# Performance work log

Hardware: AMD Instinct MI355X
Metric: run time of the kernel (lower is better)

Reference implementation:

```python
import jax, jax.numpy as jnp
import numpy as np

S, B, D, H, K, M, MEM = 1024, 2, 1024, 16, 64, 4096, 1
T = (MEM + 1) * S  # key length = (mem_len+1)*seq_len


def setup_inputs() -> dict:
    key = jax.random.key(0)
    ks = jax.random.split(key, 16)

    def w(k, shape):  # N(0, 0.02) init as in the torch module
        return jax.random.normal(k, shape, dtype=jnp.float32) * 0.02

    x = jax.random.normal(ks[0], (S, B, D), dtype=jnp.float32)
    p = jax.random.normal(ks[1], (T, B, D), dtype=jnp.float32)
    memory = jax.random.normal(ks[2], (MEM * S, B, D), dtype=jnp.float32)
    u_bias = w(ks[3], (H, K))
    v_bias = w(ks[4], (H, K))
    # Transformer-XL causal mask: query s may attend to keys t <= mem_len*S + s
    t_idx = jnp.arange(T)[None, :]
    s_idx = jnp.arange(S)[:, None]
    mask = jnp.where(t_idx <= MEM * S + s_idx, 0.0, -1e9).astype(jnp.float32)[None]  # [1,S,T]
    return {
        "x": x, "p": p, "mask": mask, "memory": memory,
        "u_bias": u_bias, "v_bias": v_bias,
        "wq_w": w(ks[5], (H * K, D)), "wke_w": w(ks[6], (H * K, D)),
        "wkr_w": w(ks[7], (H * K, D)), "wv_w": w(ks[8], (H * K, D)),
        "wc_w": w(ks[9], (D, H * K)),
        "w1_w": w(ks[10], (M, D)), "w1_b": jnp.zeros((M,), jnp.float32),
        "w2_w": w(ks[11], (D, M)), "w2_b": jnp.zeros((D,), jnp.float32),
        "ln1_g": jnp.ones((D,), jnp.float32), "ln1_b": jnp.zeros((D,), jnp.float32),
        "ln2_g": jnp.ones((D,), jnp.float32), "ln2_b": jnp.zeros((D,), jnp.float32),
    }


def _layernorm(x, g, b, eps=1e-5):
    mu = jnp.mean(x, axis=-1, keepdims=True)
    var = jnp.mean(jnp.square(x - mu), axis=-1, keepdims=True)
    return (x - mu) / jnp.sqrt(var + eps) * g + b


def reference(x, p, mask, memory, u_bias, v_bias,
              wq_w, wke_w, wkr_w, wv_w, wc_w,
              w1_w, w1_b, w2_w, w2_b, ln1_g, ln1_b, ln2_g, ln2_b):
    s_len, b_sz, d = x.shape
    q = (x @ wq_w.T).reshape(s_len, b_sz, H, K)            # [S,B,H,K]
    x_mem = jnp.concatenate([memory, x], axis=0)           # [T,B,D]
    k_e = (x_mem @ wke_w.T).reshape(T, b_sz, H, K)         # content keys
    k_r = (p @ wkr_w.T).reshape(T, b_sz, H, K)             # relative-position keys
    v = (x_mem @ wv_w.T).reshape(T, b_sz, H, K)
    # AC: content score, BD: relative-position score (Transformer-XL)
    ac = jnp.einsum("sbhk,tbhk->bhst", q + u_bias, k_e)
    bd = jnp.einsum("sbhk,tbhk->bhst", q + v_bias, k_r)
    alpha = (ac + bd) / np.sqrt(K).astype(np.float32) + mask[:, None]  # [B,H,S,T]
    alpha = jax.nn.softmax(alpha, axis=-1)
    av = jnp.einsum("bhst,tbhk->sbhk", alpha, v).reshape(s_len, b_sz, H * K)
    u = av @ wc_w.T
    u = _layernorm(u + x, ln1_g, ln1_b)
    z = jax.nn.relu(u @ w1_w.T + w1_b) @ w2_w.T + w2_b
    z = _layernorm(z + u, ln2_g, ln2_b)
    return z
```

## Files before the change

kernel.cpp:

```cpp
#include <hip/hip_runtime.h>
#include <math.h>

#define S_LEN 1024
#define BATCH 2
#define DM 1024
#define NH 16
#define HD 64
#define FFN_DIM 4096
#define T_LEN 2048
#define RQ 2048
#define RT 4096
#define KROW 72

typedef __attribute__((ext_vector_type(8))) short short8;
typedef __attribute__((ext_vector_type(4))) float f32x4;

__device__ __forceinline__ unsigned short f2bf(float f) {
    unsigned u = __builtin_bit_cast(unsigned, f);
    u += 0x7fffu + ((u >> 16) & 1u);
    return (unsigned short)(u >> 16);
}
__device__ __forceinline__ float bf2f(unsigned short s) { return __builtin_bit_cast(float, ((unsigned)s) << 16); }

#define GLD_LDS16(gptr, lptr)                                                                  \
    __builtin_amdgcn_global_load_lds((const __attribute__((address_space(1))) unsigned int*)(gptr), \
                                     (__attribute__((address_space(3))) unsigned int*)(lptr), 16, 0, 0)

__device__ __forceinline__ ushort4 cvt4(float4 v) {
    ushort4 o;
    o.x = f2bf(v.x); o.y = f2bf(v.y); o.z = f2bf(v.z); o.w = f2bf(v.w);
    return o;
}

__global__ void cast_all_kernel(const float* __restrict__ wq, const float* __restrict__ wke,
                                const float* __restrict__ wv, const float* __restrict__ wkr,
                                const float* __restrict__ wc, const float* __restrict__ w1,
                                const float* __restrict__ w2, const float* __restrict__ x,
                                const float* __restrict__ p, const float* __restrict__ mem,
                                unsigned short* __restrict__ wdst, unsigned short* __restrict__ xbf,
                                unsigned short* __restrict__ pbf, unsigned short* __restrict__ xm) {
    const long Q = 256 * 1024;
    const long W = 13 * Q;
    long i = (long)blockIdx.x * blockDim.x + threadIdx.x;
    if (i < W) {
        const float* src; long off;
        if      (i < 1 * Q) { src = wq;  off = 0; }
        else if (i < 2 * Q) { src = wke; off = 1 * Q; }
        else if (i < 3 * Q) { src = wv;  off = 2 * Q; }
        else if (i < 4 * Q) { src = wkr; off = 3 * Q; }
        else if (i < 5 * Q) { src = wc;  off = 4 * Q; }
        else if (i < 9 * Q) { src = w1;  off = 5 * Q; }
        else                { src = w2;  off = 9 * Q; }
        ((ushort4*)wdst)[i] = cvt4(((const float4*)src)[i - off]);
    } else if (i < W + 2 * Q) {
        long j = i - W;
        ((ushort4*)xbf)[j] = cvt4(((const float4*)x)[j]);
    } else if (i < W + 6 * Q) {
        long j = i - W - 2 * Q;
        ((ushort4*)pbf)[j] = cvt4(((const float4*)p)[j]);
    } else {
        long j = i - W - 6 * Q;
        float4 v = (j < 2 * Q) ? ((const float4*)mem)[j] : ((const float4*)x)[j - 2 * Q];
        ((ushort4*)xm)[j] = cvt4(v);
    }
}

#define BM 128
#define BN 64
#define BK 32

__launch_bounds__(256)
__global__ void proj_fused(const unsigned short* __restrict__ xbf, const unsigned short* __restrict__ xmbf,
                           const unsigned short* __restrict__ pbf, const unsigned short* __restrict__ wqb,
                           const unsigned short* __restrict__ wkevb, const unsigned short* __restrict__ wkrb,
                           unsigned short* __restrict__ qo, unsigned short* __restrict__ keo,
                           unsigned short* __restrict__ vTo, unsigned short* __restrict__ kro) {
    __shared__ __align__(16) short As[BM * BK];
    __shared__ __align__(16) short Bs[BN * BK];
    const int id = blockIdx.x;
    const unsigned short *A, *B;
    unsigned short *Yb, *Yv = nullptr;
    int bx, by;
    if (id < 256)       { A = xbf;  B = wqb;   Yb = qo;  bx = id & 15;  by = id >> 4; }
    else if (id < 1280) { int t = id - 256;  A = xmbf; B = wkevb; Yb = keo; Yv = vTo;
                          bx = t & 31; by = t >> 5; }
    else                { int t = id - 1280; A = pbf;  B = wkrb;  Yb = kro;
                          bx = t & 15; by = t >> 4; }
    const int tid = threadIdx.x;
    const int w = tid >> 6, lane = tid & 63;
    const int row0 = by * BM, col0 = bx * BN;
    const int wr = (w >> 1) * 64, wcn = (w & 1) * 32;
    f32x4 acc[4][2] = {};
    const int lrow = lane & 15, quad = lane >> 4;
    for (int k0 = 0; k0 < DM; k0 += BK) {
        __syncthreads();
#pragma unroll
        for (int i = 0; i < 2; ++i) {
            int c = w * 128 + i * 64 + lane;
            int row = c >> 2, kg = c & 3;
            int kl = (kg - (row >> 1)) & 3;
            GLD_LDS16(A + (long)(row0 + row) * DM + k0 + kl * 8, As + (w * 128 + i * 64) * 8);
        }
        {
            int row = tid >> 2, kg = tid & 3;
            int kl = (kg - (row >> 1)) & 3;
            GLD_LDS16(B + (long)(col0 + row) * DM + k0 + kl * 8, Bs + (w * 64) * 8);
        }
        __syncthreads();
        short8 a[4], b[2];
#pragma unroll
        for (int mi = 0; mi < 4; ++mi) {
            int r = wr + mi * 16 + lrow;
            int ph = (quad + (r >> 1)) & 3;
            a[mi] = *(const short8*)&As[r * BK + ph * 8];
        }
#pragma unroll
        for (int ni = 0; ni < 2; ++ni) {
            int r = wcn + ni * 16 + lrow;
            int ph = (quad + (r >> 1)) & 3;
            b[ni] = *(const short8*)&Bs[r * BK + ph * 8];
        }
#pragma unroll
        for (int mi = 0; mi < 4; ++mi)
#pragma unroll
            for (int ni = 0; ni < 2; ++ni)
                acc[mi][ni] = __builtin_amdgcn_mfma_f32_16x16x32_bf16(a[mi], b[ni], acc[mi][ni], 0, 0, 0);
    }
    const int mb = row0 + wr + quad * 4;
    const int nb = col0 + wcn + lrow;
    const bool iske = (col0 < 1024);
#pragma unroll
    for (int mi = 0; mi < 4; ++mi)
#pragma unroll
        for (int ni = 0; ni < 2; ++ni) {
            const int r = mb + mi * 16, cc = nb + ni * 16;
#pragma unroll
            for (int reg = 0; reg < 4; ++reg) {
                float val = acc[mi][ni][reg];
                const int rf = r + reg;
                if (Yv && !iske) {
                    int c2 = cc - 1024;
                    int t = rf >> 1, b2 = rf & 1;
                    int h2 = c2 >> 6, d2 = c2 & 63;
                    Yv[((long)(b2 * NH + h2) * HD + d2) * T_LEN + t] = f2bf(val);
                } else {
                    Yb[(long)rf * DM + cc] = f2bf(val);
                }
            }
        }
}

__launch_bounds__(256)
__global__ void gemm_mfma(const unsigned short* __restrict__ A, const unsigned short* __restrict__ B,
                          const float* __restrict__ bias, float* __restrict__ Yf,
                          unsigned short* __restrict__ Yb, int Kd, int N, int relu) {
    __shared__ __align__(16) short As[BM * BK];
    __shared__ __align__(16) short Bs[BN * BK];
    const int tid = threadIdx.x;
    const int w = tid >> 6, lane = tid & 63;
    const int row0 = blockIdx.y * BM, col0 = blockIdx.x * BN;
    const int wr = (w >> 1) * 64, wcn = (w & 1) * 32;
    f32x4 acc[4][2] = {};
    const int lrow = lane & 15, quad = lane >> 4;
    for (int k0 = 0; k0 < Kd; k0 += BK) {
        __syncthreads();
#pragma unroll
        for (int i = 0; i < 2; ++i) {
            int c = w * 128 + i * 64 + lane;
            int row = c >> 2, kg = c & 3;
            int kl = (kg - (row >> 1)) & 3;
            GLD_LDS16(A + (long)(row0 + row) * Kd + k0 + kl * 8, As + (w * 128 + i * 64) * 8);
        }
        {
            int row = tid >> 2, kg = tid & 3;
            int kl = (kg - (row >> 1)) & 3;
            GLD_LDS16(B + (long)(col0 + row) * Kd + k0 + kl * 8, Bs + (w * 64) * 8);
        }
        __syncthreads();
        short8 a[4], b[2];
#pragma unroll
        for (int mi = 0; mi < 4; ++mi) {
            int r = wr + mi * 16 + lrow;
            int ph = (quad + (r >> 1)) & 3;
            a[mi] = *(const short8*)&As[r * BK + ph * 8];
        }
#pragma unroll
        for (int ni = 0; ni < 2; ++ni) {
            int r = wcn + ni * 16 + lrow;
            int ph = (quad + (r >> 1)) & 3;
            b[ni] = *(const short8*)&Bs[r * BK + ph * 8];
        }
#pragma unroll
        for (int mi = 0; mi < 4; ++mi)
#pragma unroll
            for (int ni = 0; ni < 2; ++ni)
                acc[mi][ni] = __builtin_amdgcn_mfma_f32_16x16x32_bf16(a[mi], b[ni], acc[mi][ni], 0, 0, 0);
    }
    const int mb = row0 + wr + quad * 4;
    const int nb = col0 + wcn + lrow;
    float bb[2];
#pragma unroll
    for (int ni = 0; ni < 2; ++ni) bb[ni] = bias ? bias[nb + ni * 16] : 0.f;
#pragma unroll
    for (int mi = 0; mi < 4; ++mi)
#pragma unroll
        for (int ni = 0; ni < 2; ++ni) {
            const int r = mb + mi * 16, cc = nb + ni * 16;
#pragma unroll
            for (int reg = 0; reg < 4; ++reg) {
                float val = acc[mi][ni][reg] + bb[ni];
                if (relu) val = fmaxf(val, 0.f);
                if (Yb) Yb[(long)(r + reg) * N + cc] = f2bf(val);
                else    Yf[(long)(r + reg) * N + cc] = val;
            }
        }
}

__launch_bounds__(256)
__global__ void prep_kernel(const unsigned short* __restrict__ kr,
                            const float* __restrict__ ub, const float* __restrict__ vb,
                            unsigned short* __restrict__ ke_io, float* __restrict__ biasg) {
    const int r = blockIdx.x;
    const int tid = threadIdx.x;
    const int h = tid >> 4, seg = tid & 15;
    ushort4 keu = ((const ushort4*)(ke_io + (long)r * DM))[tid];
    ushort4 kru = ((const ushort4*)(kr + (long)r * DM))[tid];
    float ke0 = bf2f(keu.x), ke1 = bf2f(keu.y), ke2 = bf2f(keu.z), ke3 = bf2f(keu.w);
    float kr0 = bf2f(kru.x), kr1 = bf2f(kru.y), kr2 = bf2f(kru.z), kr3 = bf2f(kru.w);
    float4 u4 = ((const float4*)ub)[tid];
    float4 v4 = ((const float4*)vb)[tid];
    ushort4 s;
    s.x = f2bf((ke0 + kr0) * 0.125f); s.y = f2bf((ke1 + kr1) * 0.125f);
    s.z = f2bf((ke2 + kr2) * 0.125f); s.w = f2bf((ke3 + kr3) * 0.125f);
    ((ushort4*)(ke_io + (long)r * DM))[tid] = s;
    float part = u4.x * ke0 + u4.y * ke1 + u4.z * ke2 + u4.w * ke3
               + v4.x * kr0 + v4.y * kr1 + v4.z * kr2 + v4.w * kr3;
    part += __shfl_xor(part, 1);
    part += __shfl_xor(part, 2);
    part += __shfl_xor(part, 4);
    part += __shfl_xor(part, 8);
    if (seg == 0) {
        const int t = r >> 1, b = r & 1;
        biasg[(b * NH + h) * T_LEN + t] = part * 0.125f;
    }
}

__launch_bounds__(256)
__global__ void attn_mfma(const unsigned short* __restrict__ qg,
                          const unsigned short* __restrict__ ksum,
                          const unsigned short* __restrict__ vT,
                          const float* __restrict__ biasg,
                          unsigned short* __restrict__ avout) {
    __shared__ __align__(16) unsigned short Ks[64 * KROW];
    __shared__ __align__(16) unsigned short Vs[64 * KROW];
    __shared__ __align__(16) unsigned short Ps[4][16 * KROW];
    const int bid = blockIdx.x;
    const int stile = bid & 15, h = (bid >> 4) & 15, b = bid >> 8;
    const int tid = threadIdx.x, w = tid >> 6, lane = tid & 63;
    const int L = lane & 15, quad = lane >> 4;
    const int qbase = stile * 64 + w * 16;
    short8 qf0, qf1;
    {
        const unsigned short* qp = qg + ((long)(qbase + L) * 2 + b) * DM + h * HD + quad * 8;
        qf0 = *(const short8*)(qp);
        qf1 = *(const short8*)(qp + 32);
    }
    f32x4 O[4] = {};
    float mrow[4] = {-1e30f, -1e30f, -1e30f, -1e30f};
    float lrow[4] = {0.f, 0.f, 0.f, 0.f};
    const int nch = 17 + stile;
    const float* bias_p = biasg + (long)(b * NH + h) * T_LEN;
    const unsigned short* ks_base = ksum + (long)b * DM + h * HD;
    const unsigned short* vt_base = vT + (long)(b * NH + h) * HD * T_LEN;
    const int c0 = tid, c1 = 256 + tid;
    const int row_a = c0 >> 3, seg_a = c0 & 7;
    const int row_b = c1 >> 3, seg_b = c1 & 7;
    uint4 pk0, pk1, pv0, pv1;
    pk0 = *(const uint4*)(ks_base + (long)(0 + row_a) * 2 * DM + seg_a * 8);
    pk1 = *(const uint4*)(ks_base + (long)(0 + row_b) * 2 * DM + seg_b * 8);
    pv0 = *(const uint4*)(vt_base + (long)row_a * T_LEN + 0 + seg_a * 8);
    pv1 = *(const uint4*)(vt_base + (long)row_b * T_LEN + 0 + seg_b * 8);
    for (int ch = 0; ch < nch; ++ch) {
        const int t0 = ch * 64;
        __syncthreads();
        *(uint4*)&Ks[row_a * KROW + seg_a * 8] = pk0;
        *(uint4*)&Ks[row_b * KROW + seg_b * 8] = pk1;
        *(uint4*)&Vs[row_a * KROW + seg_a * 8] = pv0;
        *(uint4*)&Vs[row_b * KROW + seg_b * 8] = pv1;
        __syncthreads();
        if (ch + 1 < nch) {
            const int t1 = t0 + 64;
            pk0 = *(const uint4*)(ks_base + (long)(t1 + row_a) * 2 * DM + seg_a * 8);
            pk1 = *(const uint4*)(ks_base + (long)(t1 + row_b) * 2 * DM + seg_b * 8);
            pv0 = *(const uint4*)(vt_base + (long)row_a * T_LEN + t1 + seg_a * 8);
            pv1 = *(const uint4*)(vt_base + (long)row_b * T_LEN + t1 + seg_b * 8);
        }
        f32x4 S[4] = {};
#pragma unroll
        for (int kt = 0; kt < 4; ++kt) {
            short8 kb0 = *(const short8*)&Ks[(kt * 16 + L) * KROW + quad * 8];
            short8 kb1 = *(const short8*)&Ks[(kt * 16 + L) * KROW + 32 + quad * 8];
            S[kt] = __builtin_amdgcn_mfma_f32_16x16x32_bf16(qf0, kb0, S[kt], 0, 0, 0);
            S[kt] = __builtin_amdgcn_mfma_f32_16x16x32_bf16(qf1, kb1, S[kt], 0, 0, 0);
        }
        const bool lastch = (ch == nch - 1);
        float sc[4][4];
        float cm[4] = {-1e30f, -1e30f, -1e30f, -1e30f};
#pragma unroll
        for (int kt = 0; kt < 4; ++kt) {
            float bt = bias_p[t0 + kt * 16 + L];
#pragma unroll
            for (int reg = 0; reg < 4; ++reg) {
                float v = S[kt][reg] + bt;
                if (lastch && (t0 + kt * 16 + L > 1024 + qbase + quad * 4 + reg)) v = -1e30f;
                sc[kt][reg] = v;
                cm[reg] = fmaxf(cm[reg], v);
            }
        }
#pragma unroll
        for (int off = 1; off < 16; off <<= 1)
#pragma unroll
            for (int reg = 0; reg < 4; ++reg) cm[reg] = fmaxf(cm[reg], __shfl_xor(cm[reg], off));
        float cf[4];
#pragma unroll
        for (int reg = 0; reg < 4; ++reg) {
            float mn = fmaxf(mrow[reg], cm[reg]);
            cf[reg] = __expf(mrow[reg] - mn);
            mrow[reg] = mn;
            lrow[reg] *= cf[reg];
        }
        float rs[4] = {0.f, 0.f, 0.f, 0.f};
#pragma unroll
        for (int kt = 0; kt < 4; ++kt)
#pragma unroll
            for (int reg = 0; reg < 4; ++reg) {
                float pv = __expf(sc[kt][reg] - mrow[reg]);
                rs[reg] += pv;
                Ps[w][(quad * 4 + reg) * KROW + kt * 16 + L] = f2bf(pv);
            }
#pragma unroll
        for (int off = 1; off < 16; off <<= 1)
#pragma unroll
            for (int reg = 0; reg < 4; ++reg) rs[reg] += __shfl_xor(rs[reg], off);
#pragma unroll
        for (int reg = 0; reg < 4; ++reg) lrow[reg] += rs[reg];
#pragma unroll
        for (int dt = 0; dt < 4; ++dt)
#pragma unroll
            for (int reg = 0; reg < 4; ++reg) O[dt][reg] *= cf[reg];
        short8 pa0 = *(const short8*)&Ps[w][L * KROW + quad * 8];
        short8 pa1 = *(const short8*)&Ps[w][L * KROW + 32 + quad * 8];
#pragma unroll
        for (int dt = 0; dt < 4; ++dt) {
            short8 vb0 = *(const short8*)&Vs[(dt * 16 + L) * KROW + quad * 8];
            short8 vb1 = *(const short8*)&Vs[(dt * 16 + L) * KROW + 32 + quad * 8];
            O[dt] = __builtin_amdgcn_mfma_f32_16x16x32_bf16(pa0, vb0, O[dt], 0, 0, 0);
            O[dt] = __builtin_amdgcn_mfma_f32_16x16x32_bf16(pa1, vb1, O[dt], 0, 0, 0);
        }
    }
#pragma unroll
    for (int reg = 0; reg < 4; ++reg) {
        const float inv = 1.f / lrow[reg];
        const int s = qbase + quad * 4 + reg;
        unsigned short* op = avout + ((long)s * 2 + b) * DM + h * HD;
#pragma unroll
        for (int dt = 0; dt < 4; ++dt) op[dt * 16 + L] = f2bf(O[dt][reg] * inv);
    }
}

__launch_bounds__(256)
__global__ void ln_kernel(const float* __restrict__ a, const float* __restrict__ r,
                          const float* __restrict__ g, const float* __restrict__ be,
                          float* __restrict__ out, unsigned short* __restrict__ outb) {
    const int row = blockIdx.x;
    const int tid = threadIdx.x;
    float4 xa = ((const float4*)(a + (long)row * DM))[tid];
    float4 xr = ((const float4*)(r + (long)row * DM))[tid];
    float4 x = make_float4(xa.x + xr.x, xa.y + xr.y, xa.z + xr.z, xa.w + xr.w);
    float s1 = x.x + x.y + x.z + x.w;
    float s2 = x.x * x.x + x.y * x.y + x.z * x.z + x.w * x.w;
#pragma unroll
    for (int off = 32; off > 0; off >>= 1) {
        s1 += __shfl_down(s1, off);
        s2 += __shfl_down(s2, off);
    }
    __shared__ float w1s[4], w2s[4];
    const int wid = tid >> 6;
    if ((tid & 63) == 0) { w1s[wid] = s1; w2s[wid] = s2; }
    __syncthreads();
    float S1 = w1s[0] + w1s[1] + w1s[2] + w1s[3];
    float S2 = w2s[0] + w2s[1] + w2s[2] + w2s[3];
    float mu = S1 * (1.f / 1024.f);
    float var = S2 * (1.f / 1024.f) - mu * mu;
    float rstd = rsqrtf(var + 1e-5f);
    float4 gv = ((const float4*)g)[tid];
    float4 bv = ((const float4*)be)[tid];
    float4 o;
    o.x = (x.x - mu) * rstd * gv.x + bv.x;
    o.y = (x.y - mu) * rstd * gv.y + bv.y;
    o.z = (x.z - mu) * rstd * gv.z + bv.z;
    o.w = (x.w - mu) * rstd * gv.w + bv.w;
    ((float4*)(out + (long)row * DM))[tid] = o;
    if (outb) ((ushort4*)(outb + (long)row * DM))[tid] = cvt4(o);
}

extern "C" void kernel_launch(void* const* d_in, const int* in_sizes, int n_in,
                              void* d_out, int out_size, void* d_ws, size_t ws_size,
                              hipStream_t stream) {
    (void)in_sizes; (void)n_in; (void)out_size; (void)ws_size;
    const float* x    = (const float*)d_in[0];
    const float* p    = (const float*)d_in[1];
    const float* mem  = (const float*)d_in[3];
    const float* ub   = (const float*)d_in[4];
    const float* vb   = (const float*)d_in[5];
    const float* wq   = (const float*)d_in[6];
    const float* wke  = (const float*)d_in[7];
    const float* wkr  = (const float*)d_in[8];
    const float* wv   = (const float*)d_in[9];
    const float* wc   = (const float*)d_in[10];
    const float* w1   = (const float*)d_in[11];
    const float* w1b  = (const float*)d_in[12];
    const float* w2   = (const float*)d_in[13];
    const float* w2b  = (const float*)d_in[14];
    const float* ln1g = (const float*)d_in[15];
    const float* ln1b = (const float*)d_in[16];
    const float* ln2g = (const float*)d_in[17];
    const float* ln2b = (const float*)d_in[18];
    float* out = (float*)d_out;
    float* wsf = (float*)d_ws;
    unsigned short* ws16 = (unsigned short*)d_ws;

    const long HLF = 512 * 1024;
    const long M16 = 1024 * 1024;
    unsigned short* wq_bf   = ws16 + 0 * M16;
    unsigned short* wkev_bf = ws16 + 1 * M16;
    unsigned short* wkr_bf  = ws16 + 3 * M16;
    unsigned short* wc_bf   = ws16 + 4 * M16;
    unsigned short* w1_bf   = ws16 + 5 * M16;
    unsigned short* w2_bf   = ws16 + 9 * M16;
    unsigned short* x_bf   = (unsigned short*)(wsf + 13 * HLF);
    unsigned short* xm_bf  = (unsigned short*)(wsf + 15 * HLF);
    unsigned short* p_bf   = (unsigned short*)(wsf + 19 * HLF);
    unsigned short* q_bf   = (unsigned short*)(wsf + 23 * HLF);
    unsigned short* ke_bf  = (unsigned short*)(wsf + 25 * HLF);
    unsigned short* kr_bf  = (unsigned short*)(wsf + 29 * HLF);
    unsigned short* vT_bf  = (unsigned short*)(wsf + 33 * HLF);
    float* abias           = wsf + 37 * HLF;
    unsigned short* avb_bf = (unsigned short*)(wsf + 13 * HLF);
    float* t1              = wsf + 29 * HLF;
    float* u               = wsf + 25 * HLF;
    unsigned short* u_bf   = (unsigned short*)(wsf + 23 * HLF);
    unsigned short* z1_bf  = (unsigned short*)(wsf + 15 * HLF);
    float* t2              = wsf + 29 * HLF;

    cast_all_kernel<<<23552, 256, 0, stream>>>(wq, wke, wv, wkr, wc, w1, w2, x, p, mem,
                                               ws16, x_bf, p_bf, xm_bf);
    proj_fused<<<1792, 256, 0, stream>>>(x_bf, xm_bf, p_bf, wq_bf, wkev_bf, wkr_bf,
                                         q_bf, ke_bf, vT_bf, kr_bf);
    prep_kernel<<<RT, 256, 0, stream>>>(kr_bf, ub, vb, ke_bf, abias);
    attn_mfma<<<512, 256, 0, stream>>>(q_bf, ke_bf, vT_bf, abias, avb_bf);
    gemm_mfma<<<dim3(16, 16), 256, 0, stream>>>(avb_bf, wc_bf, nullptr, t1, nullptr, DM, DM, 0);
    ln_kernel<<<RQ, 256, 0, stream>>>(t1, x, ln1g, ln1b, u, u_bf);
    gemm_mfma<<<dim3(64, 16), 256, 0, stream>>>(u_bf, w1_bf, w1b, nullptr, z1_bf, DM, FFN_DIM, 1);
    gemm_mfma<<<dim3(16, 16), 256, 0, stream>>>(z1_bf, w2_bf, w2b, t2, nullptr, FFN_DIM, DM, 0);
    ln_kernel<<<RQ, 256, 0, stream>>>(t2, u, ln2g, ln2b, out, nullptr);
}
```

Before: 440.5 us.

## Split attention key range across two blocks and merge with combine kernel

The attention kernel now splits each (batch, head, query-tile) into two partitions that process interleaved 64-key chunks. Each writes unnormalized fp32 partial outputs plus running max and sum to scratch. A new combine kernel rescales and merges the two partials and writes bf16 output. This doubles the grid from 512 blocks so more of the GPU's compute units are busy, at the cost of extra global traffic for the partials, a second launch, and the causal mask check now running on every chunk.

```diff
diff --git a/kernel.cpp b/kernel.cpp
--- a/kernel.cpp
+++ b/kernel.cpp
@@ -11,6 +11,7 @@
 #define RQ 2048
 #define RT 4096
 #define KROW 72
+#define NPART 2
 
 typedef __attribute__((ext_vector_type(8))) short short8;
 typedef __attribute__((ext_vector_type(4))) float f32x4;
@@ -250,12 +251,13 @@
                           const unsigned short* __restrict__ ksum,
                           const unsigned short* __restrict__ vT,
                           const float* __restrict__ biasg,
-                          unsigned short* __restrict__ avout) {
+                          float* __restrict__ Opart, float2* __restrict__ mlout) {
     __shared__ __align__(16) unsigned short Ks[64 * KROW];
     __shared__ __align__(16) unsigned short Vs[64 * KROW];
     __shared__ __align__(16) unsigned short Ps[4][16 * KROW];
     const int bid = blockIdx.x;
-    const int stile = bid & 15, h = (bid >> 4) & 15, b = bid >> 8;
+    const int part = bid >> 9, rid = bid & 511;
+    const int stile = rid & 15, h = (rid >> 4) & 15, b = rid >> 8;
     const int tid = threadIdx.x, w = tid >> 6, lane = tid & 63;
     const int L = lane & 15, quad = lane >> 4;
     const int qbase = stile * 64 + w * 16;
@@ -276,11 +278,14 @@
     const int row_a = c0 >> 3, seg_a = c0 & 7;
     const int row_b = c1 >> 3, seg_b = c1 & 7;
     uint4 pk0, pk1, pv0, pv1;
-    pk0 = *(const uint4*)(ks_base + (long)(0 + row_a) * 2 * DM + seg_a * 8);
-    pk1 = *(const uint4*)(ks_base + (long)(0 + row_b) * 2 * DM + seg_b * 8);
-    pv0 = *(const uint4*)(vt_base + (long)row_a * T_LEN + 0 + seg_a * 8);
-    pv1 = *(const uint4*)(vt_base + (long)row_b * T_LEN + 0 + seg_b * 8);
-    for (int ch = 0; ch < nch; ++ch) {
+    {
+        const int tf = part * 64;
+        pk0 = *(const uint4*)(ks_base + (long)(tf + row_a) * 2 * DM + seg_a * 8);
+        pk1 = *(const uint4*)(ks_base + (long)(tf + row_b) * 2 * DM + seg_b * 8);
+        pv0 = *(const uint4*)(vt_base + (long)row_a * T_LEN + tf + seg_a * 8);
+        pv1 = *(const uint4*)(vt_base + (long)row_b * T_LEN + tf + seg_b * 8);
+    }
+    for (int ch = part; ch < nch; ch += NPART) {
         const int t0 = ch * 64;
         __syncthreads();
         *(uint4*)&Ks[row_a * KROW + seg_a * 8] = pk0;
@@ -288,8 +293,8 @@
         *(uint4*)&Vs[row_a * KROW + seg_a * 8] = pv0;
         *(uint4*)&Vs[row_b * KROW + seg_b * 8] = pv1;
         __syncthreads();
-        if (ch + 1 < nch) {
-            const int t1 = t0 + 64;
+        if (ch + NPART < nch) {
+            const int t1 = t0 + NPART * 64;
             pk0 = *(const uint4*)(ks_base + (long)(t1 + row_a) * 2 * DM + seg_a * 8);
             pk1 = *(const uint4*)(ks_base + (long)(t1 + row_b) * 2 * DM + seg_b * 8);
             pv0 = *(const uint4*)(vt_base + (long)row_a * T_LEN + t1 + seg_a * 8);
@@ -303,7 +308,6 @@
             S[kt] = __builtin_amdgcn_mfma_f32_16x16x32_bf16(qf0, kb0, S[kt], 0, 0, 0);
             S[kt] = __builtin_amdgcn_mfma_f32_16x16x32_bf16(qf1, kb1, S[kt], 0, 0, 0);
         }
-        const bool lastch = (ch == nch - 1);
         float sc[4][4];
         float cm[4] = {-1e30f, -1e30f, -1e30f, -1e30f};
 #pragma unroll
@@ -312,7 +316,7 @@
 #pragma unroll
             for (int reg = 0; reg < 4; ++reg) {
                 float v = S[kt][reg] + bt;
-                if (lastch && (t0 + kt * 16 + L > 1024 + qbase + quad * 4 + reg)) v = -1e30f;
+                if (t0 + kt * 16 + L > 1024 + qbase + quad * 4 + reg) v = -1e30f;
                 sc[kt][reg] = v;
                 cm[reg] = fmaxf(cm[reg], v);
             }
@@ -358,14 +362,39 @@
             O[dt] = __builtin_amdgcn_mfma_f32_16x16x32_bf16(pa1, vb1, O[dt], 0, 0, 0);
         }
     }
+    const long rbase = ((long)(part * 2 + b) * NH + h) * S_LEN;
 #pragma unroll
     for (int reg = 0; reg < 4; ++reg) {
-        const float inv = 1.f / lrow[reg];
         const int s = qbase + quad * 4 + reg;
-        unsigned short* op = avout + ((long)s * 2 + b) * DM + h * HD;
-#pragma unroll
-        for (int dt = 0; dt < 4; ++dt) op[dt * 16 + L] = f2bf(O[dt][reg] * inv);
-    }
+        float* op = Opart + (rbase + s) * 64;
+#pragma unroll
+        for (int dt = 0; dt < 4; ++dt) op[dt * 16 + L] = O[dt][reg];
+        if (L == 0) mlout[rbase + s] = make_float2(mrow[reg], lrow[reg]);
+    }
+}
+
+__launch_bounds__(256)
+__global__ void attn_combine(const float* __restrict__ Opart, const float2* __restrict__ ml,
+                             unsigned short* __restrict__ avout) {
+    const int i = blockIdx.x * 256 + threadIdx.x;
+    const int d4 = i & 15;
+    const int row = i >> 4;
+    const int s = row & 1023;
+    const int bh = row >> 10;
+    const int b = bh >> 4, h = bh & 15;
+    float2 ml0 = ml[row], ml1 = ml[row + 32768];
+    float m = fmaxf(ml0.x, ml1.x);
+    float a0 = __expf(ml0.x - m), a1 = __expf(ml1.x - m);
+    float inv = 1.f / (a0 * ml0.y + a1 * ml1.y);
+    a0 *= inv; a1 *= inv;
+    float4 o0 = ((const float4*)Opart)[(long)row * 16 + d4];
+    float4 o1 = ((const float4*)Opart)[((long)row + 32768) * 16 + d4];
+    float4 o;
+    o.x = a0 * o0.x + a1 * o1.x;
+    o.y = a0 * o0.y + a1 * o1.y;
+    o.z = a0 * o0.z + a1 * o1.z;
+    o.w = a0 * o0.w + a1 * o1.w;
+    *(ushort4*)(avout + ((long)s * 2 + b) * DM + h * HD + d4 * 4) = cvt4(o);
 }
 
 __launch_bounds__(256)
@@ -446,6 +475,8 @@
     unsigned short* kr_bf  = (unsigned short*)(wsf + 29 * HLF);
     unsigned short* vT_bf  = (unsigned short*)(wsf + 33 * HLF);
     float* abias           = wsf + 37 * HLF;
+    float* Opart           = wsf + 15 * HLF;
+    float2* mlpart         = (float2*)(wsf + 29 * HLF);
     unsigned short* avb_bf = (unsigned short*)(wsf + 13 * HLF);
     float* t1              = wsf + 29 * HLF;
     float* u               = wsf + 25 * HLF;
@@ -458,7 +489,8 @@
     proj_fused<<<1792, 256, 0, stream>>>(x_bf, xm_bf, p_bf, wq_bf, wkev_bf, wkr_bf,
                                          q_bf, ke_bf, vT_bf, kr_bf);
     prep_kernel<<<RT, 256, 0, stream>>>(kr_bf, ub, vb, ke_bf, abias);
-    attn_mfma<<<512, 256, 0, stream>>>(q_bf, ke_bf, vT_bf, abias, avb_bf);
+    attn_mfma<<<512 * NPART, 256, 0, stream>>>(q_bf, ke_bf, vT_bf, abias, Opart, mlpart);
+    attn_combine<<<2048, 256, 0, stream>>>(Opart, mlpart, avb_bf);
     gemm_mfma<<<dim3(16, 16), 256, 0, stream>>>(avb_bf, wc_bf, nullptr, t1, nullptr, DM, DM, 0);
     ln_kernel<<<RQ, 256, 0, stream>>>(t1, x, ln1g, ln1b, u, u_bf);
     gemm_mfma<<<dim3(64, 16), 256, 0, stream>>>(u_bf, w1_bf, w1b, nullptr, z1_bf, DM, FFN_DIM, 1);
```

New measurement: 425.2 us. -3.5%, faster.
